# Kernel tuning notes

Hardware: AMD Instinct MI355X
Metric: run time of the kernel (lower is better)

Reference implementation:

```python
import jax, jax.numpy as jnp
import numpy as np

B, S, D, H = 16, 2048, 2048, 16
HD = D // H
PROJ = D  # proj_ratio = 1.0
PAD_ID = 50257
LN_EPS = 1e-5
MASKED_BIAS = -1e9


def setup_inputs() -> dict:
    key = jax.random.key(0)
    ks = jax.random.split(key, 12)
    sc = 0.02
    return {
        "hidden_states": jax.random.normal(ks[0], (B, S, D), dtype=jnp.float32),
        "input_ids_with_pads": jax.random.randint(ks[1], (B, S), 0, PAD_ID, dtype=jnp.int64),
        "ln_w": jnp.ones((D,), jnp.float32),
        "ln_b": jnp.zeros((D,), jnp.float32),
        "wq": sc * jax.random.normal(ks[2], (D, D), jnp.float32),
        "bq": jnp.zeros((D,), jnp.float32),
        "wk": sc * jax.random.normal(ks[3], (D, D), jnp.float32),
        "bk": jnp.zeros((D,), jnp.float32),
        "wv": sc * jax.random.normal(ks[4], (D, D), jnp.float32),
        "bv": jnp.zeros((D,), jnp.float32),
        "wo": sc * jax.random.normal(ks[5], (D, PROJ), jnp.float32),
        "bo": jnp.zeros((PROJ,), jnp.float32),
    }


def _layernorm(x, g, b):
    mu = jnp.mean(x, axis=-1, keepdims=True)
    var = jnp.mean(jnp.square(x - mu), axis=-1, keepdims=True)
    return (x - mu) * jax.lax.rsqrt(var + LN_EPS) * g + b


def _last_token_index(tokens):
    # select_at_last_token: argmax of cumsum of the non-pad mask == index of
    # the last non-pad token (first index where the cumsum reaches its max).
    mask = (tokens != PAD_ID).astype(jnp.int32)
    return jnp.argmax(jnp.cumsum(mask, axis=1), axis=1)  # [B]


def reference(hidden_states, input_ids_with_pads, ln_w, ln_b,
              wq, bq, wk, bk, wv, bv, wo, bo):
    x = _layernorm(hidden_states, ln_w, ln_b)  # [B,S,D]
    idx = _last_token_index(input_ids_with_pads)
    # Efficient gather instead of the original index_select + diagonal trick.
    x_last = x[jnp.arange(B), idx]  # [B,D]

    q = (x_last @ wq + bq).reshape(B, H, HD)          # single query per batch
    k = (x @ wk + bk).reshape(B, S, H, HD).transpose(0, 2, 1, 3)  # [B,H,S,HD]
    v = (x @ wv + bv).reshape(B, S, H, HD).transpose(0, 2, 1, 3)  # [B,H,S,HD]

    # GPT-Neo _attn: compute in float32, NO 1/sqrt(head_dim) scaling.
    # Causal mask for query at position key_length-1 covers the full key range,
    # i.e. it is all-True here, so it is a no-op (kept implicit).
    w = jnp.einsum("bhd,bhsd->bhs", q.astype(jnp.float32), k.astype(jnp.float32))
    w = jax.nn.softmax(w, axis=-1).astype(v.dtype)    # [B,H,S]
    attn = jnp.einsum("bhs,bhsd->bhd", w, v)          # [B,H,HD]
    attn = attn.reshape(B, D)                          # merge heads
    out = attn @ wo + bo                               # [B,PROJ]
    return out
```

## Files before the change

### kernel.cpp

```cpp
#include <hip/hip_runtime.h>
#include <hip/hip_bf16.h>

#define BB 16
#define SS 2048
#define DD 2048
#define HH 16
#define HDIM 128
#define PAD_ID 50257
#define LN_EPS 1e-5f

__device__ __forceinline__ float block_sum256(float v, float* s4) {
    #pragma unroll
    for (int m = 32; m >= 1; m >>= 1) v += __shfl_xor(v, m, 64);
    __syncthreads();
    if ((threadIdx.x & 63) == 0) s4[threadIdx.x >> 6] = v;
    __syncthreads();
    return s4[0] + s4[1] + s4[2] + s4[3];
}
__device__ __forceinline__ float block_max256(float v, float* s4) {
    #pragma unroll
    for (int m = 32; m >= 1; m >>= 1) v = fmaxf(v, __shfl_xor(v, m, 64));
    __syncthreads();
    if ((threadIdx.x & 63) == 0) s4[threadIdx.x >> 6] = v;
    __syncthreads();
    return fmaxf(fmaxf(s4[0], s4[1]), fmaxf(s4[2], s4[3]));
}

__global__ __launch_bounds__(256) void k_prep(const float* __restrict__ hid, const int* __restrict__ ids,
                                              const float* __restrict__ g, const float* __restrict__ be,
                                              float* __restrict__ xlast) {
    int b = blockIdx.x, t = threadIdx.x;
    __shared__ int sm[256];
    __shared__ float s4[4];
    const int* row = ids + (size_t)b * SS;
    int best = -1;
    for (int s = t; s < SS; s += 256)
        if (row[s] != PAD_ID) best = s;
    sm[t] = best;
    __syncthreads();
    for (int off = 128; off > 0; off >>= 1) {
        if (t < off) sm[t] = max(sm[t], sm[t + off]);
        __syncthreads();
    }
    int idx = (sm[0] < 0) ? 0 : sm[0];
    const float4* row4 = (const float4*)(hid + ((size_t)b * SS + idx) * DD);
    float4 v0 = row4[t], v1 = row4[t + 256];
    float s  = v0.x + v0.y + v0.z + v0.w + v1.x + v1.y + v1.z + v1.w;
    float sq = v0.x*v0.x + v0.y*v0.y + v0.z*v0.z + v0.w*v0.w
             + v1.x*v1.x + v1.y*v1.y + v1.z*v1.z + v1.w*v1.w;
    s  = block_sum256(s, s4);
    sq = block_sum256(sq, s4);
    float mu = s * (1.0f / DD);
    float rstd = rsqrtf(sq * (1.0f / DD) - mu * mu + LN_EPS);
    const float4* g4 = (const float4*)g;
    const float4* b4 = (const float4*)be;
    float4 ga = g4[t], gb = g4[t + 256], ba = b4[t], bb = b4[t + 256];
    float4 o0, o1;
    o0.x = (v0.x - mu) * rstd * ga.x + ba.x;  o0.y = (v0.y - mu) * rstd * ga.y + ba.y;
    o0.z = (v0.z - mu) * rstd * ga.z + ba.z;  o0.w = (v0.w - mu) * rstd * ga.w + ba.w;
    o1.x = (v1.x - mu) * rstd * gb.x + bb.x;  o1.y = (v1.y - mu) * rstd * gb.y + bb.y;
    o1.z = (v1.z - mu) * rstd * gb.z + bb.z;  o1.w = (v1.w - mu) * rstd * gb.w + bb.w;
    ((float4*)(xlast + (size_t)b * DD))[t]       = o0;
    ((float4*)(xlast + (size_t)b * DD))[t + 256] = o1;
}

__global__ __launch_bounds__(256) void k_init3(float* __restrict__ q, float* __restrict__ attn,
                                               float* __restrict__ out, const float* __restrict__ bq,
                                               const float* __restrict__ bv, const float* __restrict__ bo) {
    int i = blockIdx.x * 256 + threadIdx.x;
    int which = blockIdx.y;
    float* dst = which == 0 ? q : (which == 1 ? attn : out);
    const float* bias = which == 0 ? bq : (which == 1 ? bv : bo);
    dst[i] = bias[i & (DD - 1)];
}

__global__ __launch_bounds__(256) void k_q(const float* __restrict__ xlast, const float* __restrict__ wq,
                                           float* __restrict__ q) {
    int ptile = blockIdx.x, kch = blockIdx.y, tid = threadIdx.x;
    __shared__ float xs[16][64];
    {
        int b = tid >> 4, c4 = tid & 15;
        *(float4*)&xs[b][c4 * 4] = *(const float4*)&xlast[(size_t)b * DD + kch * 64 + c4 * 4];
    }
    __syncthreads();
    int p = ptile * 256 + tid;
    float acc[16];
    #pragma unroll
    for (int b = 0; b < 16; b++) acc[b] = 0.f;
    for (int dd = 0; dd < 64; dd++) {
        float wqv = wq[(size_t)(kch * 64 + dd) * DD + p];
        #pragma unroll
        for (int b = 0; b < 16; b++) acc[b] = fmaf(xs[b][dd], wqv, acc[b]);
    }
    #pragma unroll
    for (int b = 0; b < 16; b++) atomicAdd(&q[(size_t)b * DD + p], acc[b]);
}

__global__ __launch_bounds__(256) void k_t(const float* __restrict__ wk, const float* __restrict__ q,
                                           const float* __restrict__ g, float* __restrict__ t_out,
                                           float* __restrict__ tg_out) {
    int d = blockIdx.x, tid = threadIdx.x;
    __shared__ float wkl[16 * 132];
    #pragma unroll
    for (int k = 0; k < 2; k++) {
        int f4 = tid + k * 256;
        int h = f4 >> 5, j4 = f4 & 31;
        *(float4*)&wkl[h * 132 + j4 * 4] = *(const float4*)&wk[(size_t)d * DD + h * 128 + j4 * 4];
    }
    __syncthreads();
    int b = tid >> 4, h = tid & 15;
    const float4* q4 = (const float4*)(q + (size_t)b * DD + h * 128);
    float acc = 0.f;
    #pragma unroll
    for (int j4 = 0; j4 < 32; j4++) {
        float4 qv = q4[j4];
        float4 wv4 = *(const float4*)&wkl[h * 132 + j4 * 4];
        acc = fmaf(qv.x, wv4.x, fmaf(qv.y, wv4.y, fmaf(qv.z, wv4.z, fmaf(qv.w, wv4.w, acc))));
    }
    size_t o = (size_t)(b * 16 + h) * DD + d;
    t_out[o] = acc;
    tg_out[o] = acc * g[d];
}

__global__ __launch_bounds__(256) void k_G(const float* __restrict__ t_in, const float* __restrict__ tg_in,
                                           const float* __restrict__ q, const float* __restrict__ lnb,
                                           const float* __restrict__ bk, float* __restrict__ G1,
                                           float* __restrict__ wconst) {
    int bh = blockIdx.x, tid = threadIdx.x;
    int b = bh >> 4, h = bh & 15;
    __shared__ float s4[4];
    const float4* tg4 = (const float4*)(tg_in + (size_t)bh * DD);
    const float4* t4  = (const float4*)(t_in + (size_t)bh * DD);
    const float4* lb4 = (const float4*)lnb;
    float g1p = 0.f, g2p = 0.f;
    #pragma unroll
    for (int k = 0; k < 2; k++) {
        int f = tid + k * 256;
        float4 a = tg4[f];
        g1p += a.x + a.y + a.z + a.w;
        float4 tv = t4[f];
        float4 bv = lb4[f];
        g2p = fmaf(tv.x, bv.x, fmaf(tv.y, bv.y, fmaf(tv.z, bv.z, fmaf(tv.w, bv.w, g2p))));
    }
    float cp = 0.f;
    if (tid < 128) cp = bk[h * 128 + tid] * q[(size_t)b * DD + h * 128 + tid];
    float G1v = block_sum256(g1p, s4);
    float rest = block_sum256(g2p + cp, s4);
    if (tid == 0) { G1[bh] = G1v; wconst[bh] = rest; }
}

__global__ __launch_bounds__(256) void k_logits4(const float* __restrict__ hid, const float* __restrict__ tg,
                                                 const float* __restrict__ G1, const float* __restrict__ wcst,
                                                 float* __restrict__ wout, float* __restrict__ muA,
                                                 float* __restrict__ rsA) {
    int b = blockIdx.x, st = blockIdx.y;
    int tid = threadIdx.x, qd = tid & 15, rg = tid >> 4;
    __shared__ float tl[2][16][132];
    __shared__ float red[256 * 17];
    const size_t rowbase = ((size_t)b * SS + st * 32 + rg * 2) * DD;
    const float* tgb = tg + (size_t)b * 16 * DD;

    float raw[2][16], sum[2], ssq[2];
    #pragma unroll
    for (int r = 0; r < 2; r++) {
        sum[r] = 0.f; ssq[r] = 0.f;
        #pragma unroll
        for (int h = 0; h < 16; h++) raw[r][h] = 0.f;
    }

    float4 xa[2][2], xb[2][2], ta[2], tb[2];

    #pragma unroll
    for (int k = 0; k < 2; k++) {
        int f = tid + k * 256; int h = f >> 5, c4 = f & 31;
        ta[k] = *(const float4*)&tgb[(size_t)h * DD + c4 * 4];
    }
    #pragma unroll
    for (int rr = 0; rr < 2; rr++)
        #pragma unroll
        for (int k = 0; k < 2; k++)
            xa[rr][k] = *(const float4*)&hid[rowbase + (size_t)rr * DD + (qd + 16 * k) * 4];
    #pragma unroll
    for (int k = 0; k < 2; k++) {
        int f = tid + k * 256; int h = f >> 5, c4 = f & 31;
        *(float4*)&tl[0][h][c4 * 4] = ta[k];
    }
    __syncthreads();

    auto do_chunk = [&](int c, int buf, float4 (&xc)[2][2], float4 (&xn)[2][2], float4 (&tn)[2]) {
        const bool last = (c == 15);
        if (!last) {
            int d0n = (c + 1) * 128;
            #pragma unroll
            for (int k = 0; k < 2; k++) {
                int f = tid + k * 256; int h = f >> 5, c4 = f & 31;
                tn[k] = *(const float4*)&tgb[(size_t)h * DD + d0n + c4 * 4];
            }
            #pragma unroll
            for (int rr = 0; rr < 2; rr++)
                #pragma unroll
                for (int k = 0; k < 2; k++)
                    xn[rr][k] = *(const float4*)&hid[rowbase + (size_t)rr * DD + d0n + (qd + 16 * k) * 4];
        }
        #pragma unroll
        for (int k = 0; k < 2; k++) {
            #pragma unroll
            for (int h = 0; h < 16; h++) {
                float4 tv = *(const float4*)&tl[buf][h][(qd + 16 * k) * 4];
                float4 x0 = xc[0][k], x1 = xc[1][k];
                raw[0][h] = fmaf(x0.x, tv.x, fmaf(x0.y, tv.y, fmaf(x0.z, tv.z, fmaf(x0.w, tv.w, raw[0][h]))));
                raw[1][h] = fmaf(x1.x, tv.x, fmaf(x1.y, tv.y, fmaf(x1.z, tv.z, fmaf(x1.w, tv.w, raw[1][h]))));
            }
            #pragma unroll
            for (int rr = 0; rr < 2; rr++) {
                float4 x = xc[rr][k];
                sum[rr] += x.x + x.y + x.z + x.w;
                ssq[rr] = fmaf(x.x, x.x, fmaf(x.y, x.y, fmaf(x.z, x.z, fmaf(x.w, x.w, ssq[rr]))));
            }
        }
        if (!last) {
            #pragma unroll
            for (int k = 0; k < 2; k++) {
                int f = tid + k * 256; int h = f >> 5, c4 = f & 31;
                *(float4*)&tl[buf ^ 1][h][c4 * 4] = tn[k];
            }
        }
        __syncthreads();
    };

    #pragma unroll 1
    for (int cc = 0; cc < 8; cc++) {
        do_chunk(2 * cc,     0, xa, xb, tb);
        do_chunk(2 * cc + 1, 1, xb, xa, ta);
    }

    #pragma unroll
    for (int m = 1; m < 16; m <<= 1) {
        #pragma unroll
        for (int r = 0; r < 2; r++) {
            sum[r] += __shfl_xor(sum[r], m, 64);
            ssq[r] += __shfl_xor(ssq[r], m, 64);
        }
    }

    float g1 = G1[b * 16 + qd];
    float wc = wcst[b * 16 + qd];
    __syncthreads();
    #pragma unroll
    for (int rr = 0; rr < 2; rr++) {
        #pragma unroll
        for (int h = 0; h < 16; h++) red[tid * 17 + h] = raw[rr][h];
        __syncthreads();
        float tot = 0.f;
        #pragma unroll
        for (int j = 0; j < 16; j++) tot += red[(rg * 16 + j) * 17 + qd];
        int s = st * 32 + rg * 2 + rr;
        float mu = sum[rr] * (1.0f / DD);
        float rstd = rsqrtf(ssq[rr] * (1.0f / DD) - mu * mu + LN_EPS);
        wout[(size_t)(b * 16 + qd) * SS + s] = rstd * (tot - mu * g1) + wc;
        if (qd == 0) { muA[(size_t)b * SS + s] = mu; rsA[(size_t)b * SS + s] = rstd; }
        __syncthreads();
    }
}

__global__ __launch_bounds__(256) void k_softmax(const float* __restrict__ wlog, const float* __restrict__ muA,
                                                 const float* __restrict__ rsA, float* __restrict__ coef,
                                                 float* __restrict__ Mout) {
    int bh = blockIdx.x, tid = threadIdx.x;
    int b = bh >> 4;
    __shared__ float s4[4];
    const float4* w4 = (const float4*)(wlog + (size_t)bh * SS);
    float4 v0 = w4[tid], v1 = w4[tid + 256];
    float mx = fmaxf(fmaxf(fmaxf(v0.x, v0.y), fmaxf(v0.z, v0.w)),
                     fmaxf(fmaxf(v1.x, v1.y), fmaxf(v1.z, v1.w)));
    mx = block_max256(mx, s4);
    float4 e0, e1;
    e0.x = __expf(v0.x - mx); e0.y = __expf(v0.y - mx); e0.z = __expf(v0.z - mx); e0.w = __expf(v0.w - mx);
    e1.x = __expf(v1.x - mx); e1.y = __expf(v1.y - mx); e1.z = __expf(v1.z - mx); e1.w = __expf(v1.w - mx);
    float ssum = e0.x + e0.y + e0.z + e0.w + e1.x + e1.y + e1.z + e1.w;
    ssum = block_sum256(ssum, s4);
    float inv = 1.0f / ssum;
    const float4* r4 = (const float4*)(rsA + (size_t)b * SS);
    const float4* m4 = (const float4*)(muA + (size_t)b * SS);
    float4 ra = r4[tid], rb = r4[tid + 256], ma = m4[tid], mb = m4[tid + 256];
    float4 c0, c1;
    c0.x = e0.x * inv * ra.x; c0.y = e0.y * inv * ra.y; c0.z = e0.z * inv * ra.z; c0.w = e0.w * inv * ra.w;
    c1.x = e1.x * inv * rb.x; c1.y = e1.y * inv * rb.y; c1.z = e1.z * inv * rb.z; c1.w = e1.w * inv * rb.w;
    ((float4*)(coef + (size_t)bh * SS))[tid] = c0;
    ((float4*)(coef + (size_t)bh * SS))[tid + 256] = c1;
    float Mp = c0.x * ma.x + c0.y * ma.y + c0.z * ma.z + c0.w * ma.w
             + c1.x * mb.x + c1.y * mb.y + c1.z * mb.z + c1.w * mb.w;
    Mp = block_sum256(Mp, s4);
    if (tid == 0) Mout[bh] = Mp;
}

__global__ __launch_bounds__(256) void k_pv3(const float* __restrict__ hid, const float* __restrict__ coef,
                                             float* __restrict__ Apart) {
    int b = blockIdx.x, dt = blockIdx.y, ch = blockIdx.z, tid = threadIdx.x;
    __shared__ float cl[128][16];
    int s0 = ch * 128;
    #pragma unroll
    for (int k = 0; k < 2; k++) {
        int f = tid + k * 256; int h = f >> 5, s4i = f & 31;
        float4 c4 = *(const float4*)&coef[(size_t)(b * 16 + h) * SS + s0 + s4i * 4];
        cl[s4i * 4 + 0][h] = c4.x; cl[s4i * 4 + 1][h] = c4.y;
        cl[s4i * 4 + 2][h] = c4.z; cl[s4i * 4 + 3][h] = c4.w;
    }
    __syncthreads();
    int d = dt * 1024 + tid * 4;
    const float* hb = hid + ((size_t)b * SS + s0) * DD + d;
    float4 acc[16];
    #pragma unroll
    for (int h = 0; h < 16; h++) acc[h] = make_float4(0.f, 0.f, 0.f, 0.f);
    float4 xv[4];
    #pragma unroll
    for (int i = 0; i < 4; i++) xv[i] = *(const float4*)(hb + (size_t)i * DD);
    #pragma unroll 1
    for (int sb = 0; sb < 32; sb++) {
        #pragma unroll
        for (int i = 0; i < 4; i++) {
            int s = sb * 4 + i;
            float4 x = xv[i];
            if (sb < 31) xv[i] = *(const float4*)(hb + (size_t)(s + 4) * DD);
            float4 ca = *(const float4*)&cl[s][0];
            float4 cb = *(const float4*)&cl[s][4];
            float4 cc = *(const float4*)&cl[s][8];
            float4 cd = *(const float4*)&cl[s][12];
            acc[0].x = fmaf(ca.x, x.x, acc[0].x); acc[0].y = fmaf(ca.x, x.y, acc[0].y);
            acc[0].z = fmaf(ca.x, x.z, acc[0].z); acc[0].w = fmaf(ca.x, x.w, acc[0].w);
            acc[1].x = fmaf(ca.y, x.x, acc[1].x); acc[1].y = fmaf(ca.y, x.y, acc[1].y);
            acc[1].z = fmaf(ca.y, x.z, acc[1].z); acc[1].w = fmaf(ca.y, x.w, acc[1].w);
            acc[2].x = fmaf(ca.z, x.x, acc[2].x); acc[2].y = fmaf(ca.z, x.y, acc[2].y);
            acc[2].z = fmaf(ca.z, x.z, acc[2].z); acc[2].w = fmaf(ca.z, x.w, acc[2].w);
            acc[3].x = fmaf(ca.w, x.x, acc[3].x); acc[3].y = fmaf(ca.w, x.y, acc[3].y);
            acc[3].z = fmaf(ca.w, x.z, acc[3].z); acc[3].w = fmaf(ca.w, x.w, acc[3].w);
            acc[4].x = fmaf(cb.x, x.x, acc[4].x); acc[4].y = fmaf(cb.x, x.y, acc[4].y);
            acc[4].z = fmaf(cb.x, x.z, acc[4].z); acc[4].w = fmaf(cb.x, x.w, acc[4].w);
            acc[5].x = fmaf(cb.y, x.x, acc[5].x); acc[5].y = fmaf(cb.y, x.y, acc[5].y);
            acc[5].z = fmaf(cb.y, x.z, acc[5].z); acc[5].w = fmaf(cb.y, x.w, acc[5].w);
            acc[6].x = fmaf(cb.z, x.x, acc[6].x); acc[6].y = fmaf(cb.z, x.y, acc[6].y);
            acc[6].z = fmaf(cb.z, x.z, acc[6].z); acc[6].w = fmaf(cb.z, x.w, acc[6].w);
            acc[7].x = fmaf(cb.w, x.x, acc[7].x); acc[7].y = fmaf(cb.w, x.y, acc[7].y);
            acc[7].z = fmaf(cb.w, x.z, acc[7].z); acc[7].w = fmaf(cb.w, x.w, acc[7].w);
            acc[8].x = fmaf(cc.x, x.x, acc[8].x); acc[8].y = fmaf(cc.x, x.y, acc[8].y);
            acc[8].z = fmaf(cc.x, x.z, acc[8].z); acc[8].w = fmaf(cc.x, x.w, acc[8].w);
            acc[9].x = fmaf(cc.y, x.x, acc[9].x); acc[9].y = fmaf(cc.y, x.y, acc[9].y);
            acc[9].z = fmaf(cc.y, x.z, acc[9].z); acc[9].w = fmaf(cc.y, x.w, acc[9].w);
            acc[10].x = fmaf(cc.z, x.x, acc[10].x); acc[10].y = fmaf(cc.z, x.y, acc[10].y);
            acc[10].z = fmaf(cc.z, x.z, acc[10].z); acc[10].w = fmaf(cc.z, x.w, acc[10].w);
            acc[11].x = fmaf(cc.w, x.x, acc[11].x); acc[11].y = fmaf(cc.w, x.y, acc[11].y);
            acc[11].z = fmaf(cc.w, x.z, acc[11].z); acc[11].w = fmaf(cc.w, x.w, acc[11].w);
            acc[12].x = fmaf(cd.x, x.x, acc[12].x); acc[12].y = fmaf(cd.x, x.y, acc[12].y);
            acc[12].z = fmaf(cd.x, x.z, acc[12].z); acc[12].w = fmaf(cd.x, x.w, acc[12].w);
            acc[13].x = fmaf(cd.y, x.x, acc[13].x); acc[13].y = fmaf(cd.y, x.y, acc[13].y);
            acc[13].z = fmaf(cd.y, x.z, acc[13].z); acc[13].w = fmaf(cd.y, x.w, acc[13].w);
            acc[14].x = fmaf(cd.z, x.x, acc[14].x); acc[14].y = fmaf(cd.z, x.y, acc[14].y);
            acc[14].z = fmaf(cd.z, x.z, acc[14].z); acc[14].w = fmaf(cd.z, x.w, acc[14].w);
            acc[15].x = fmaf(cd.w, x.x, acc[15].x); acc[15].y = fmaf(cd.w, x.y, acc[15].y);
            acc[15].z = fmaf(cd.w, x.z, acc[15].z); acc[15].w = fmaf(cd.w, x.w, acc[15].w);
        }
    }
    #pragma unroll
    for (int h = 0; h < 16; h++)
        *(float4*)&Apart[((size_t)(ch * 16 + b) * 16 + h) * DD + d] = acc[h];
}

__global__ __launch_bounds__(256) void k_red(const float* __restrict__ Apart, float* __restrict__ A) {
    size_t i4 = (size_t)blockIdx.x * 256 + threadIdx.x;
    const float4* ap = (const float4*)Apart;
    float4 acc = make_float4(0.f, 0.f, 0.f, 0.f);
    #pragma unroll
    for (int c = 0; c < 16; c++) {
        float4 v = ap[(size_t)c * 131072 + i4];
        acc.x += v.x; acc.y += v.y; acc.z += v.z; acc.w += v.w;
    }
    ((float4*)A)[i4] = acc;
}

__global__ __launch_bounds__(256) void k_attnv(const float* __restrict__ A, const float* __restrict__ M,
                                               const float* __restrict__ g, const float* __restrict__ be,
                                               const float* __restrict__ wv, float* __restrict__ attn) {
    int h = blockIdx.x, dc = blockIdx.y, tid = threadIdx.x;
    __shared__ float yl[16][64];
    int d0 = dc * 64;
    {
        int b = tid >> 4, c4 = tid & 15;
        float4 a4 = *(const float4*)&A[(size_t)(b * 16 + h) * DD + d0 + c4 * 4];
        float4 g4 = *(const float4*)&g[d0 + c4 * 4];
        float4 b4 = *(const float4*)&be[d0 + c4 * 4];
        float m = M[b * 16 + h];
        float4 y;
        y.x = g4.x * (a4.x - m) + b4.x;  y.y = g4.y * (a4.y - m) + b4.y;
        y.z = g4.z * (a4.z - m) + b4.z;  y.w = g4.w * (a4.w - m) + b4.w;
        *(float4*)&yl[b][c4 * 4] = y;
    }
    __syncthreads();
    int j = tid & 127, h2 = tid >> 7;
    float acc[16];
    #pragma unroll
    for (int b = 0; b < 16; b++) acc[b] = 0.f;
    for (int dl = 0; dl < 32; dl++) {
        int dd = h2 * 32 + dl;
        float wvv = wv[(size_t)(d0 + dd) * DD + h * 128 + j];
        #pragma unroll
        for (int b = 0; b < 16; b++) acc[b] = fmaf(yl[b][dd], wvv, acc[b]);
    }
    #pragma unroll
    for (int b = 0; b < 16; b++) atomicAdd(&attn[(size_t)b * DD + h * 128 + j], acc[b]);
}

__global__ __launch_bounds__(256) void k_out(const float* __restrict__ attn, const float* __restrict__ wo,
                                             float* __restrict__ out) {
    int ptile = blockIdx.x, cch = blockIdx.y, tid = threadIdx.x;
    __shared__ float al[16][64];
    int c0 = cch * 64;
    {
        int b = tid >> 4, c4 = tid & 15;
        *(float4*)&al[b][c4 * 4] = *(const float4*)&attn[(size_t)b * DD + c0 + c4 * 4];
    }
    __syncthreads();
    int p = ptile * 256 + tid;
    float acc[16];
    #pragma unroll
    for (int b = 0; b < 16; b++) acc[b] = 0.f;
    for (int cc = 0; cc < 64; cc++) {
        float wov = wo[(size_t)(c0 + cc) * DD + p];
        #pragma unroll
        for (int b = 0; b < 16; b++) acc[b] = fmaf(al[b][cc], wov, acc[b]);
    }
    #pragma unroll
    for (int b = 0; b < 16; b++) atomicAdd(&out[(size_t)b * DD + p], acc[b]);
}

extern "C" void kernel_launch(void* const* d_in, const int* in_sizes, int n_in,
                              void* d_out, int out_size, void* d_ws, size_t ws_size,
                              hipStream_t stream) {
    const float* hid = (const float*)d_in[0];
    const int*   ids = (const int*)d_in[1];
    const float* lnw = (const float*)d_in[2];
    const float* lnb = (const float*)d_in[3];
    const float* wq  = (const float*)d_in[4];
    const float* bq  = (const float*)d_in[5];
    const float* wk  = (const float*)d_in[6];
    const float* bk  = (const float*)d_in[7];
    const float* wv  = (const float*)d_in[8];
    const float* bv  = (const float*)d_in[9];
    const float* wo  = (const float*)d_in[10];
    const float* bo  = (const float*)d_in[11];
    float* out = (float*)d_out;

    float* ws = (float*)d_ws;
    float* xlast = ws;
    float* q     = xlast + 32768;
    float* t     = q + 32768;
    float* tg    = t + 524288;
    float* G1    = tg + 524288;
    float* wcst  = G1 + 256;
    float* wlog  = wcst + 256;
    float* muA   = wlog + 524288;
    float* rsA   = muA + 32768;
    float* coef  = rsA + 32768;
    float* Mbh   = coef + 524288;
    float* Abh   = Mbh + 256;
    float* attn  = Abh + 524288;
    float* Apart = attn + 32768;

    k_prep<<<16, 256, 0, stream>>>(hid, ids, lnw, lnb, xlast);
    k_init3<<<dim3(128, 3), 256, 0, stream>>>(q, attn, out, bq, bv, bo);
    k_q<<<dim3(8, 32), 256, 0, stream>>>(xlast, wq, q);
    k_t<<<2048, 256, 0, stream>>>(wk, q, lnw, t, tg);
    k_G<<<256, 256, 0, stream>>>(t, tg, q, lnb, bk, G1, wcst);
    k_logits4<<<dim3(16, 64), 256, 0, stream>>>(hid, tg, G1, wcst, wlog, muA, rsA);
    k_softmax<<<256, 256, 0, stream>>>(wlog, muA, rsA, coef, Mbh);
    k_pv3<<<dim3(16, 2, 16), 256, 0, stream>>>(hid, coef, Apart);
    k_red<<<512, 256, 0, stream>>>(Apart, Abh);
    k_attnv<<<dim3(16, 32), 256, 0, stream>>>(Abh, Mbh, lnw, lnb, wv, attn);
    k_out<<<dim3(8, 32), 256, 0, stream>>>(attn, wo, out);
}
```

Baseline: 250.1 us.

## Split logits kernel across hidden dimension halves with separate fixup reduction kernel

The logits kernel now splits the 2048-wide hidden dimension into two halves across a new grid z dimension. This doubles the block count, and the kernel writes partial dot products plus row sum and sum-of-squares into a workspace. A new small kernel combines the two halves, computes the LayerNorm mean and rstd, and writes the logits. The shared reduction buffer is aliased onto the tile buffer to cut LDS use, and launch bounds ask for 3 blocks per CU to raise occupancy. The cost is an extra launch plus partial-result traffic to global memory.

```diff
diff --git a/kernel.cpp b/kernel.cpp
--- a/kernel.cpp
+++ b/kernel.cpp
@@ -149,14 +149,12 @@
     if (tid == 0) { G1[bh] = G1v; wconst[bh] = rest; }
 }
 
-__global__ __launch_bounds__(256) void k_logits4(const float* __restrict__ hid, const float* __restrict__ tg,
-                                                 const float* __restrict__ G1, const float* __restrict__ wcst,
-                                                 float* __restrict__ wout, float* __restrict__ muA,
-                                                 float* __restrict__ rsA) {
-    int b = blockIdx.x, st = blockIdx.y;
+__global__ __launch_bounds__(256, 3) void k_logits5(const float* __restrict__ hid, const float* __restrict__ tg,
+                                                    float* __restrict__ part) {
+    int b = blockIdx.x, st = blockIdx.y, dh = blockIdx.z;
     int tid = threadIdx.x, qd = tid & 15, rg = tid >> 4;
-    __shared__ float tl[2][16][132];
-    __shared__ float red[256 * 17];
+    __shared__ float tl[2 * 16 * 136];
+    const int d0base = dh * 1024;
     const size_t rowbase = ((size_t)b * SS + st * 32 + rg * 2) * DD;
     const float* tgb = tg + (size_t)b * 16 * DD;
 
@@ -173,24 +171,24 @@
     #pragma unroll
     for (int k = 0; k < 2; k++) {
         int f = tid + k * 256; int h = f >> 5, c4 = f & 31;
-        ta[k] = *(const float4*)&tgb[(size_t)h * DD + c4 * 4];
+        ta[k] = *(const float4*)&tgb[(size_t)h * DD + d0base + c4 * 4];
     }
     #pragma unroll
     for (int rr = 0; rr < 2; rr++)
         #pragma unroll
         for (int k = 0; k < 2; k++)
-            xa[rr][k] = *(const float4*)&hid[rowbase + (size_t)rr * DD + (qd + 16 * k) * 4];
+            xa[rr][k] = *(const float4*)&hid[rowbase + (size_t)rr * DD + d0base + (qd + 16 * k) * 4];
     #pragma unroll
     for (int k = 0; k < 2; k++) {
         int f = tid + k * 256; int h = f >> 5, c4 = f & 31;
-        *(float4*)&tl[0][h][c4 * 4] = ta[k];
+        *(float4*)&tl[h * 136 + c4 * 4] = ta[k];
     }
     __syncthreads();
 
     auto do_chunk = [&](int c, int buf, float4 (&xc)[2][2], float4 (&xn)[2][2], float4 (&tn)[2]) {
-        const bool last = (c == 15);
+        const bool last = (c == 7);
         if (!last) {
-            int d0n = (c + 1) * 128;
+            int d0n = d0base + (c + 1) * 128;
             #pragma unroll
             for (int k = 0; k < 2; k++) {
                 int f = tid + k * 256; int h = f >> 5, c4 = f & 31;
@@ -206,7 +204,7 @@
         for (int k = 0; k < 2; k++) {
             #pragma unroll
             for (int h = 0; h < 16; h++) {
-                float4 tv = *(const float4*)&tl[buf][h][(qd + 16 * k) * 4];
+                float4 tv = *(const float4*)&tl[buf * 2176 + h * 136 + (qd + 16 * k) * 4];
                 float4 x0 = xc[0][k], x1 = xc[1][k];
                 raw[0][h] = fmaf(x0.x, tv.x, fmaf(x0.y, tv.y, fmaf(x0.z, tv.z, fmaf(x0.w, tv.w, raw[0][h]))));
                 raw[1][h] = fmaf(x1.x, tv.x, fmaf(x1.y, tv.y, fmaf(x1.z, tv.z, fmaf(x1.w, tv.w, raw[1][h]))));
@@ -222,17 +220,20 @@
             #pragma unroll
             for (int k = 0; k < 2; k++) {
                 int f = tid + k * 256; int h = f >> 5, c4 = f & 31;
-                *(float4*)&tl[buf ^ 1][h][c4 * 4] = tn[k];
+                *(float4*)&tl[(buf ^ 1) * 2176 + h * 136 + c4 * 4] = tn[k];
             }
         }
         __syncthreads();
     };
 
-    #pragma unroll 1
-    for (int cc = 0; cc < 8; cc++) {
-        do_chunk(2 * cc,     0, xa, xb, tb);
-        do_chunk(2 * cc + 1, 1, xb, xa, ta);
-    }
+    do_chunk(0, 0, xa, xb, tb);
+    do_chunk(1, 1, xb, xa, ta);
+    do_chunk(2, 0, xa, xb, tb);
+    do_chunk(3, 1, xb, xa, ta);
+    do_chunk(4, 0, xa, xb, tb);
+    do_chunk(5, 1, xb, xa, ta);
+    do_chunk(6, 0, xa, xb, tb);
+    do_chunk(7, 1, xb, xa, ta);
 
     #pragma unroll
     for (int m = 1; m < 16; m <<= 1) {
@@ -243,11 +244,10 @@
         }
     }
 
-    float g1 = G1[b * 16 + qd];
-    float wc = wcst[b * 16 + qd];
-    __syncthreads();
+    float* red = tl;
     #pragma unroll
     for (int rr = 0; rr < 2; rr++) {
+        __syncthreads();
         #pragma unroll
         for (int h = 0; h < 16; h++) red[tid * 17 + h] = raw[rr][h];
         __syncthreads();
@@ -255,11 +255,28 @@
         #pragma unroll
         for (int j = 0; j < 16; j++) tot += red[(rg * 16 + j) * 17 + qd];
         int s = st * 32 + rg * 2 + rr;
-        float mu = sum[rr] * (1.0f / DD);
-        float rstd = rsqrtf(ssq[rr] * (1.0f / DD) - mu * mu + LN_EPS);
-        wout[(size_t)(b * 16 + qd) * SS + s] = rstd * (tot - mu * g1) + wc;
-        if (qd == 0) { muA[(size_t)b * SS + s] = mu; rsA[(size_t)b * SS + s] = rstd; }
-        __syncthreads();
+        float* p = part + ((size_t)(b * 2 + dh) * SS + s) * 20;
+        p[qd] = tot;
+        if (qd == 0) { p[16] = sum[rr]; p[17] = ssq[rr]; }
+    }
+}
+
+__global__ __launch_bounds__(256) void k_lfix(const float* __restrict__ part, const float* __restrict__ G1,
+                                              const float* __restrict__ wcst, float* __restrict__ wout,
+                                              float* __restrict__ muA, float* __restrict__ rsA) {
+    int b = blockIdx.x;
+    int s = blockIdx.y * 256 + threadIdx.x;
+    const float* p0 = part + ((size_t)(b * 2 + 0) * SS + s) * 20;
+    const float* p1 = part + ((size_t)(b * 2 + 1) * SS + s) * 20;
+    float sum = p0[16] + p1[16], ssq = p0[17] + p1[17];
+    float mu = sum * (1.0f / DD);
+    float rstd = rsqrtf(ssq * (1.0f / DD) - mu * mu + LN_EPS);
+    muA[(size_t)b * SS + s] = mu;
+    rsA[(size_t)b * SS + s] = rstd;
+    #pragma unroll
+    for (int h = 0; h < 16; h++) {
+        float raw = p0[h] + p1[h];
+        wout[(size_t)(b * 16 + h) * SS + s] = rstd * (raw - mu * G1[b * 16 + h]) + wcst[b * 16 + h];
     }
 }
 
@@ -464,13 +481,15 @@
     float* Abh   = Mbh + 256;
     float* attn  = Abh + 524288;
     float* Apart = attn + 32768;
+    float* part  = Apart + 8388608;
 
     k_prep<<<16, 256, 0, stream>>>(hid, ids, lnw, lnb, xlast);
     k_init3<<<dim3(128, 3), 256, 0, stream>>>(q, attn, out, bq, bv, bo);
     k_q<<<dim3(8, 32), 256, 0, stream>>>(xlast, wq, q);
     k_t<<<2048, 256, 0, stream>>>(wk, q, lnw, t, tg);
     k_G<<<256, 256, 0, stream>>>(t, tg, q, lnb, bk, G1, wcst);
-    k_logits4<<<dim3(16, 64), 256, 0, stream>>>(hid, tg, G1, wcst, wlog, muA, rsA);
+    k_logits5<<<dim3(16, 64, 2), 256, 0, stream>>>(hid, tg, part);
+    k_lfix<<<dim3(16, 8), 256, 0, stream>>>(part, G1, wcst, wlog, muA, rsA);
     k_softmax<<<256, 256, 0, stream>>>(wlog, muA, rsA, coef, Mbh);
     k_pv3<<<dim3(16, 2, 16), 256, 0, stream>>>(hid, coef, Apart);
     k_red<<<512, 256, 0, stream>>>(Apart, Abh);
```

New measurement: 553.9 us. 2.21x slower.
